# Performance work log

Measured on AMD Instinct MI355X. Metric: run time of the kernel, lower is better.

The kernel has to match this reference:

```python
import jax, jax.numpy as jnp
import numpy as np
import math

FACTOR = 5

def setup_inputs() -> dict:
    key = jax.random.key(0)
    k1, k2, k3, k4 = jax.random.split(key, 4)
    B, L, H, D = 4, 4096, 8, 64
    sample_k = min(FACTOR * int(np.ceil(np.log(L))), L)  # 45
    return {
        "queries": jax.random.normal(k1, (B, L, H, D), dtype=jnp.float32),
        "keys": jax.random.normal(k2, (B, L, H, D), dtype=jnp.float32),
        "values": jax.random.normal(k3, (B, L, H, D), dtype=jnp.float32),
        "index_sample": jax.random.randint(k4, (L, sample_k), 0, L, dtype=jnp.int64),
    }

def reference(queries, keys, values, index_sample):
    # [B, L, H, D] -> [B, H, L, D]
    Q = jnp.transpose(queries, (0, 2, 1, 3))
    K = jnp.transpose(keys, (0, 2, 1, 3))
    V = jnp.transpose(values, (0, 2, 1, 3))
    b, h, l_q, d = Q.shape
    l_k = K.shape[2]

    # n_top (u) per Informer: factor * ceil(ln(l_q)), capped at l_q
    u = min(FACTOR * int(math.ceil(math.log(l_q))), l_q)

    # --- _prob_QK: sampled QK scores ---
    # K_sample: [b, h, l_q, sample_k, d] via shared per-query random sample
    K_sample = K[:, :, index_sample, :]
    # Q_K_sample: [b, h, l_q, sample_k]
    Q_K_sample = jnp.einsum("bhqd,bhqsd->bhqs", Q, K_sample)
    # sparsity measure M: max - mean(sum/l_k)
    M = Q_K_sample.max(axis=-1) - Q_K_sample.sum(axis=-1) / l_k
    # top-u queries (indices; order irrelevant to the math)
    _, M_top = jax.lax.top_k(M, u)  # [b, h, u]

    # Q_reduce: [b, h, u, d]
    Q_reduce = jnp.take_along_axis(Q, M_top[..., None], axis=2)
    # full scores for selected queries: [b, h, u, l_k]
    scale = 1.0 / math.sqrt(d)
    scores_top = jnp.einsum("bhud,bhkd->bhuk", Q_reduce, K) * scale

    # --- initial context: mean of V broadcast over queries ---
    context = jnp.broadcast_to(V.mean(axis=2, keepdims=True), (b, h, l_q, d))

    # --- update context at selected query positions ---
    attn = jax.nn.softmax(scores_top, axis=-1)          # [b, h, u, l_k]
    upd = jnp.einsum("bhuk,bhkd->bhud", attn, V)         # [b, h, u, d]
    bi = jnp.arange(b)[:, None, None]
    hi = jnp.arange(h)[None, :, None]
    context = context.at[bi, hi, M_top].set(upd)

    # [B, H, L, D] -> [B, L, H, D]
    return jnp.transpose(context, (0, 2, 1, 3))
```

## Files before the change

kernel.cpp:

```cpp
#include <hip/hip_runtime.h>
#include <stdint.h>

#define B_ 4
#define L_ 4096
#define H_ 8
#define D_ 64
#define S_ 45
#define U_ 45
#define BH_ 32
#define KC_ 16
#define STRIDE_ (H_*D_)
#define BSTR_ ((size_t)L_*H_*D_)

__device__ __forceinline__ bool detect_idx64(const int* idxp){
    bool z = true;
    #pragma unroll
    for (int i = 1; i < 32; i += 2) z = z && (idxp[i] == 0);
    return z;
}

typedef float v4f_ __attribute__((ext_vector_type(4)));
__device__ __forceinline__ float4 ntload4(const float4* p){
    v4f_ v = __builtin_nontemporal_load((const v4f_*)p);
    return make_float4(v.x, v.y, v.z, v.w);
}
__device__ __forceinline__ void ntstore4(float4* p, float4 f){
    v4f_ v; v.x = f.x; v.y = f.y; v.z = f.z; v.w = f.w;
    __builtin_nontemporal_store(v, (v4f_*)p);
}

__global__ __launch_bounds__(256) void kM(const float* __restrict__ Qb,
                                          const float* __restrict__ Kb,
                                          const int* __restrict__ idxp,
                                          float* __restrict__ Mout){
    int g = blockIdx.x;
    int grp8 = g & 7;
    int b  = grp8 >> 1;
    int hg = grp8 & 1;
    int chunk = g >> 3;
    int q0 = chunk * 16;
    bool idx64 = detect_idx64(idxp);

    __shared__ int lidx[16*S_];
    for (int i = threadIdx.x; i < 16*S_; i += 256)
        lidx[i] = idx64 ? __builtin_nontemporal_load(&idxp[2*(q0*S_ + i)])
                        : __builtin_nontemporal_load(&idxp[q0*S_ + i]);
    __syncthreads();

    int lane = threadIdx.x & 63;
    int w    = threadIdx.x >> 6;
    int grp  = lane >> 4;
    int l16  = lane & 15;
    int ql   = w*4 + grp;
    int q    = q0 + ql;

    const float4* qr = (const float4*)(Qb + (size_t)b*BSTR_ + (size_t)q*STRIDE_ + hg*256);
    float4 qf0 = ntload4(qr + l16);
    float4 qf1 = ntload4(qr + 16 + l16);
    float4 qf2 = ntload4(qr + 32 + l16);
    float4 qf3 = ntload4(qr + 48 + l16);

    const float* kbase = Kb + (size_t)b*BSTR_ + hg*256;
    float mxa = -1e30f, mxb = -1e30f, sma = 0.f, smb = 0.f;
    const int* myIdx = &lidx[ql*S_];

    #pragma unroll 3
    for (int s = 0; s < S_; s++){
        int ki = myIdx[s];
        const float4* kr = (const float4*)(kbase + (size_t)ki*STRIDE_);
        float4 k0 = kr[l16], k1 = kr[16+l16], k2 = kr[32+l16], k3 = kr[48+l16];
        float p0 = qf0.x*k0.x; p0 = fmaf(qf0.y,k0.y,p0); p0 = fmaf(qf0.z,k0.z,p0); p0 = fmaf(qf0.w,k0.w,p0);
        float p1 = qf1.x*k1.x; p1 = fmaf(qf1.y,k1.y,p1); p1 = fmaf(qf1.z,k1.z,p1); p1 = fmaf(qf1.w,k1.w,p1);
        float p2 = qf2.x*k2.x; p2 = fmaf(qf2.y,k2.y,p2); p2 = fmaf(qf2.z,k2.z,p2); p2 = fmaf(qf2.w,k2.w,p2);
        float p3 = qf3.x*k3.x; p3 = fmaf(qf3.y,k3.y,p3); p3 = fmaf(qf3.z,k3.z,p3); p3 = fmaf(qf3.w,k3.w,p3);
        float u0 = p0 + __shfl_xor(p0, 8);
        float u1 = p1 + __shfl_xor(p1, 8);
        float u2 = p2 + __shfl_xor(p2, 8);
        float u3 = p3 + __shfl_xor(p3, 8);
        float va = (l16 < 8) ? u0 : u2;
        float vb = (l16 < 8) ? u1 : u3;
        #pragma unroll
        for (int off = 1; off < 8; off <<= 1){
            va += __shfl_xor(va, off);
            vb += __shfl_xor(vb, off);
        }
        mxa = fmaxf(mxa, va); sma += va;
        mxb = fmaxf(mxb, vb); smb += vb;
    }
    int hsel = (l16==0) ? 0 : (l16==1) ? 1 : (l16==8) ? 2 : (l16==9) ? 3 : -1;
    if (hsel >= 0){
        float mv = (l16 & 1) ? mxb : mxa;
        float sv = (l16 & 1) ? smb : sma;
        __builtin_nontemporal_store(mv - sv*(1.0f/L_),
            &Mout[(size_t)(b*8 + hg*4 + hsel)*L_ + q]);
    }
}

__global__ __launch_bounds__(512) void kTopF(const float* __restrict__ M,
                                             int* __restrict__ Mtop,
                                             float* __restrict__ meanZ,
                                             unsigned short* __restrict__ selRow16){
    int bh = blockIdx.x;
    int t = threadIdx.x;
    if (t < 64) meanZ[bh*64 + t] = 0.f;
    for (int j = t; j < L_; j += 512) selRow16[(size_t)bh*L_ + j] = 0;

    __shared__ float cV[8*U_];
    __shared__ int   cI[8*U_];
    int wv = t >> 6, lane = t & 63;
    const float* Mr = M + (size_t)bh*L_ + wv*512;
    float v[8];
    #pragma unroll
    for (int j = 0; j < 8; j++) v[j] = Mr[lane + 64*j];

    for (int it = 0; it < U_; it++){
        float best = -1e30f; int bidx = 0x7fffffff;
        #pragma unroll
        for (int j = 0; j < 8; j++){
            int id = lane + 64*j;
            if (v[j] > best){ best = v[j]; bidx = id; }
        }
        #pragma unroll
        for (int off = 1; off < 64; off <<= 1){
            float ov = __shfl_xor(best, off); int oi = __shfl_xor(bidx, off);
            if (ov > best || (ov == best && oi < bidx)){ best = ov; bidx = oi; }
        }
        if (lane == 0){ cV[wv*U_ + it] = best; cI[wv*U_ + it] = wv*512 + bidx; }
        if (lane == (bidx & 63)) v[bidx >> 6] = -1e30f;
    }
    __syncthreads();
    if (t < 64){
        float v2[6]; int id2[6];
        #pragma unroll
        for (int j = 0; j < 6; j++){
            int slot = t + 64*j;
            if (slot < 8*U_){ v2[j] = cV[slot]; id2[j] = cI[slot]; }
            else            { v2[j] = -1e30f;  id2[j] = 0x7fffffff; }
        }
        for (int it = 0; it < U_; it++){
            float best = -1e30f; int bidx = 0x7fffffff; int bj = 0;
            #pragma unroll
            for (int j = 0; j < 6; j++){
                if (v2[j] > best || (v2[j] == best && id2[j] < bidx)){
                    best = v2[j]; bidx = id2[j]; bj = j;
                }
            }
            float myBest = best; int myIdx = bidx;
            #pragma unroll
            for (int off = 1; off < 64; off <<= 1){
                float ov = __shfl_xor(best, off); int oi = __shfl_xor(bidx, off);
                if (ov > best || (ov == best && oi < bidx)){ best = ov; bidx = oi; }
            }
            if (t == 0){
                Mtop[bh*U_ + it] = bidx;
                selRow16[(size_t)bh*L_ + bidx] = (unsigned short)(it + 1);
            }
            if (myBest == best && myIdx == bidx) v2[bj] = -1e30f;
        }
    }
}

__global__ __launch_bounds__(256) void kAttnPart(const float* __restrict__ Qb,
                                                 const float* __restrict__ Kb,
                                                 const float* __restrict__ Vb,
                                                 const int*   __restrict__ Mtop,
                                                 float* __restrict__ Opart,
                                                 float* __restrict__ mlG,
                                                 float* __restrict__ mean){
    int bh = blockIdx.y, b = bh >> 3, h = bh & 7;
    int kc = blockIdx.x, uh = blockIdx.z;
    int u0 = uh ? 23 : 0;
    int nu = uh ? 22 : 23;
    int t = threadIdx.x;
    __shared__ float S[24][260];
    __shared__ int   qidx[23];

    if (t < nu) qidx[t] = Mtop[bh*U_ + u0 + t];
    for (int i = t; i < (24 - nu)*260; i += 256) (&S[nu][0])[i] = 0.f;
    __syncthreads();

    int k = kc*256 + t;
    float4 kf[16];
    const float4* K4 = (const float4*)(Kb + (size_t)b*BSTR_ + (size_t)k*STRIDE_ + h*D_);
    #pragma unroll
    for (int c = 0; c < 16; c++) kf[c] = K4[c];
    for (int u = 0; u < nu; u++){
        int qi = __builtin_amdgcn_readfirstlane(qidx[u]);
        const float4* qp = (const float4*)(Qb + (size_t)b*BSTR_ + (size_t)qi*STRIDE_ + h*D_);
        float a0=0.f, a1=0.f, a2=0.f, a3=0.f;
        #pragma unroll
        for (int c = 0; c < 16; c++){
            float4 qv = qp[c];
            a0 = fmaf(qv.x, kf[c].x, a0);
            a1 = fmaf(qv.y, kf[c].y, a1);
            a2 = fmaf(qv.z, kf[c].z, a2);
            a3 = fmaf(qv.w, kf[c].w, a3);
        }
        S[u][t] = ((a0+a1)+(a2+a3)) * 0.125f;
    }
    __syncthreads();

    int wv = t >> 6, lane = t & 63;
    for (int u = wv; u < nu; u += 4){
        float4 sv = *(const float4*)&S[u][lane*4];
        float m = fmaxf(fmaxf(sv.x, sv.y), fmaxf(sv.z, sv.w));
        #pragma unroll
        for (int off = 1; off < 64; off <<= 1) m = fmaxf(m, __shfl_xor(m, off));
        float e0 = __expf(sv.x - m), e1 = __expf(sv.y - m);
        float e2 = __expf(sv.z - m), e3 = __expf(sv.w - m);
        float ls = (e0+e1)+(e2+e3);
        #pragma unroll
        for (int off = 1; off < 64; off <<= 1) ls += __shfl_xor(ls, off);
        float4 pv; pv.x = e0; pv.y = e1; pv.z = e2; pv.w = e3;
        *(float4*)&S[u][lane*4] = pv;
        if (lane == 0){
            size_t mi = ((size_t)(bh*KC_ + kc)*U_ + u0 + u)*2;
            mlG[mi] = m; mlG[mi+1] = ls;
        }
    }
    __syncthreads();

    int d = lane, w = wv;
    int ub = w*6;
    int nuw = nu - ub; if (nuw > 6) nuw = 6; if (nuw < 0) nuw = 0;
    float acc[6];
    #pragma unroll
    for (int j = 0; j < 6; j++) acc[j] = 0.f;
    float vsum = 0.f;
    const float* Vbase = Vb + (size_t)b*BSTR_ + (size_t)(kc*256)*STRIDE_ + h*D_ + d;
    for (int kb = 0; kb < 64; kb++){
        float v0 = Vbase[(size_t)(kb*4+0)*STRIDE_];
        float v1 = Vbase[(size_t)(kb*4+1)*STRIDE_];
        float v2 = Vbase[(size_t)(kb*4+2)*STRIDE_];
        float v3 = Vbase[(size_t)(kb*4+3)*STRIDE_];
        if (uh == 0 && w == 0) vsum += (v0+v1)+(v2+v3);
        #pragma unroll
        for (int j = 0; j < 6; j++){
            float4 p = *(const float4*)&S[ub+j][kb*4];
            acc[j] = fmaf(p.x, v0, acc[j]);
            acc[j] = fmaf(p.y, v1, acc[j]);
            acc[j] = fmaf(p.z, v2, acc[j]);
            acc[j] = fmaf(p.w, v3, acc[j]);
        }
    }
    for (int j = 0; j < nuw; j++)
        Opart[((size_t)(bh*KC_ + kc)*U_ + u0 + ub + j)*64 + d] = acc[j];
    if (uh == 0 && w == 0)
        atomicAdd(&mean[bh*64 + d], vsum);
}

__global__ __launch_bounds__(256) void kOut(const float* __restrict__ mean,
                                            const unsigned short* __restrict__ selRow16,
                                            const float* __restrict__ mlG,
                                            const float* __restrict__ Opart,
                                            float* __restrict__ out){
    size_t t = (size_t)blockIdx.x*256 + threadIdx.x;
    int d16 = (int)(t & 15); int h = (int)((t >> 4) & 7);
    int l   = (int)((t >> 7) & 4095); int b = (int)(t >> 19);
    int bh = b*8 + h;
    int sel = selRow16[(size_t)bh*L_ + l];
    float4 o;
    if (sel == 0){
        o = *(const float4*)(mean + bh*64 + d16*4);
        const float inv = 1.0f / L_;
        o.x *= inv; o.y *= inv; o.z *= inv; o.w *= inv;
    } else {
        int u = sel - 1;
        float mstar = -1e30f;
        #pragma unroll
        for (int kc = 0; kc < KC_; kc++)
            mstar = fmaxf(mstar, mlG[((size_t)(bh*KC_ + kc)*U_ + u)*2]);
        float lsum = 0.f;
        float4 acc; acc.x = acc.y = acc.z = acc.w = 0.f;
        #pragma unroll
        for (int kc = 0; kc < KC_; kc++){
            size_t mi = ((size_t)(bh*KC_ + kc)*U_ + u)*2;
            float wgt = __expf(mlG[mi] - mstar);
            lsum = fmaf(mlG[mi+1], wgt, lsum);
            float4 op = *(const float4*)(Opart + ((size_t)(bh*KC_ + kc)*U_ + u)*64 + d16*4);
            acc.x = fmaf(wgt, op.x, acc.x);
            acc.y = fmaf(wgt, op.y, acc.y);
            acc.z = fmaf(wgt, op.z, acc.z);
            acc.w = fmaf(wgt, op.w, acc.w);
        }
        float inv = 1.0f / lsum;
        acc.x *= inv; acc.y *= inv; acc.z *= inv; acc.w *= inv;
        o = acc;
    }
    ntstore4(((float4*)out) + t, o);
}

extern "C" void kernel_launch(void* const* d_in, const int* in_sizes, int n_in,
                              void* d_out, int out_size, void* d_ws, size_t ws_size,
                              hipStream_t stream) {
    const float* Qb  = (const float*)d_in[0];
    const float* Kb  = (const float*)d_in[1];
    const float* Vb  = (const float*)d_in[2];
    const int*   idx = (const int*)d_in[3];
    float* out = (float*)d_out;

    float* ws = (float*)d_ws;
    float* M      = ws;
    int*   Mtop   = (int*)(ws + 131072);
    float* mean   = ws + 133120;
    unsigned short* selRow16 = (unsigned short*)(ws + 135168);
    float* mlG    = ws + 266240;
    float* Opart  = ws + 315392;

    kM        <<<dim3(2048),       dim3(256), 0, stream>>>(Qb, Kb, idx, M);
    kTopF     <<<dim3(32),         dim3(512), 0, stream>>>(M, Mtop, mean, selRow16);
    kAttnPart <<<dim3(KC_, 32, 2), dim3(256), 0, stream>>>(Qb, Kb, Vb, Mtop, Opart, mlG, mean);
    kOut      <<<dim3(8192),       dim3(256), 0, stream>>>(mean, selRow16, mlG, Opart, out);
}
```

Baseline: 307.4 us.

## Split top-k into per-segment kernel and parallel rank-based merge

The single 32-block top-k kernel becomes two kernels. First, 256 one-wave blocks each pick the top 45 of a 512-element segment. Second, a merge kernel ranks all 360 candidates in parallel by binary-searching the other sorted lists, replacing the serial 45-iteration wave reduction. This spreads the selection across more CUs and shortens the serial merge, at the cost of an extra launch and a global round trip for the candidates.

Result: faster. 276.8 us (-9.9%).

```diff
diff --git a/kernel.cpp b/kernel.cpp
--- a/kernel.cpp
+++ b/kernel.cpp
@@ -96,66 +96,71 @@
     }
 }
 
-__global__ __launch_bounds__(512) void kTopF(const float* __restrict__ M,
-                                             int* __restrict__ Mtop,
-                                             float* __restrict__ meanZ,
-                                             unsigned short* __restrict__ selRow16){
+__global__ __launch_bounds__(64) void kTopSeg(const float* __restrict__ M,
+                                              float* __restrict__ candV,
+                                              int*   __restrict__ candI,
+                                              unsigned short* __restrict__ selRow16){
+    int g = blockIdx.x;
+    int bh = g >> 3, seg = g & 7;
+    int lane = threadIdx.x;
+    uint4 z; z.x = z.y = z.z = z.w = 0u;
+    ((uint4*)(selRow16 + (size_t)bh*L_ + seg*512))[lane] = z;
+
+    const float* Mr = M + (size_t)bh*L_ + seg*512;
+    float v[8];
+    #pragma unroll
+    for (int j = 0; j < 8; j++) v[j] = Mr[lane + 64*j];
+
+    float* cV = candV + (size_t)g*U_;
+    int*   cI = candI + (size_t)g*U_;
+    for (int it = 0; it < U_; it++){
+        float best = -1e30f; int bidx = 0x7fffffff;
+        #pragma unroll
+        for (int j = 0; j < 8; j++){
+            int id = lane + 64*j;
+            if (v[j] > best){ best = v[j]; bidx = id; }
+        }
+        #pragma unroll
+        for (int off = 1; off < 64; off <<= 1){
+            float ov = __shfl_xor(best, off); int oi = __shfl_xor(bidx, off);
+            if (ov > best || (ov == best && oi < bidx)){ best = ov; bidx = oi; }
+        }
+        if (lane == 0){ cV[it] = best; cI[it] = seg*512 + bidx; }
+        if (lane == (bidx & 63)) v[bidx >> 6] = -1e30f;
+    }
+}
+
+__global__ __launch_bounds__(384) void kTopMerge(const float* __restrict__ candV,
+                                                 const int*   __restrict__ candI,
+                                                 int* __restrict__ Mtop,
+                                                 unsigned short* __restrict__ selRow16,
+                                                 float* __restrict__ meanZ){
     int bh = blockIdx.x;
     int t = threadIdx.x;
     if (t < 64) meanZ[bh*64 + t] = 0.f;
-    for (int j = t; j < L_; j += 512) selRow16[(size_t)bh*L_ + j] = 0;
-
-    __shared__ float cV[8*U_];
-    __shared__ int   cI[8*U_];
-    int wv = t >> 6, lane = t & 63;
-    const float* Mr = M + (size_t)bh*L_ + wv*512;
-    float v[8];
-    #pragma unroll
-    for (int j = 0; j < 8; j++) v[j] = Mr[lane + 64*j];
-
-    for (int it = 0; it < U_; it++){
-        float best = -1e30f; int bidx = 0x7fffffff;
-        #pragma unroll
-        for (int j = 0; j < 8; j++){
-            int id = lane + 64*j;
-            if (v[j] > best){ best = v[j]; bidx = id; }
-        }
-        #pragma unroll
-        for (int off = 1; off < 64; off <<= 1){
-            float ov = __shfl_xor(best, off); int oi = __shfl_xor(bidx, off);
-            if (ov > best || (ov == best && oi < bidx)){ best = ov; bidx = oi; }
-        }
-        if (lane == 0){ cV[wv*U_ + it] = best; cI[wv*U_ + it] = wv*512 + bidx; }
-        if (lane == (bidx & 63)) v[bidx >> 6] = -1e30f;
-    }
-    __syncthreads();
-    if (t < 64){
-        float v2[6]; int id2[6];
-        #pragma unroll
-        for (int j = 0; j < 6; j++){
-            int slot = t + 64*j;
-            if (slot < 8*U_){ v2[j] = cV[slot]; id2[j] = cI[slot]; }
-            else            { v2[j] = -1e30f;  id2[j] = 0x7fffffff; }
-        }
-        for (int it = 0; it < U_; it++){
-            float best = -1e30f; int bidx = 0x7fffffff; int bj = 0;
-            #pragma unroll
-            for (int j = 0; j < 6; j++){
-                if (v2[j] > best || (v2[j] == best && id2[j] < bidx)){
-                    best = v2[j]; bidx = id2[j]; bj = j;
-                }
+    __shared__ float sV[8*U_];
+    __shared__ int   sI[8*U_];
+    if (t < 8*U_){ sV[t] = candV[(size_t)bh*8*U_ + t]; sI[t] = candI[(size_t)bh*8*U_ + t]; }
+    __syncthreads();
+    if (t < 8*U_){
+        int s = t / U_, r = t - s*U_;
+        float v = sV[t]; int gi = sI[t];
+        int rank = r;
+        for (int s2 = 0; s2 < 8; s2++){
+            if (s2 == s) continue;
+            const float* LV = &sV[s2*U_];
+            const int*   LI = &sI[s2*U_];
+            int lo = 0, hi = U_;
+            while (lo < hi){
+                int mid = (lo + hi) >> 1;
+                bool before = (LV[mid] > v) || (LV[mid] == v && LI[mid] < gi);
+                if (before) lo = mid + 1; else hi = mid;
             }
-            float myBest = best; int myIdx = bidx;
-            #pragma unroll
-            for (int off = 1; off < 64; off <<= 1){
-                float ov = __shfl_xor(best, off); int oi = __shfl_xor(bidx, off);
-                if (ov > best || (ov == best && oi < bidx)){ best = ov; bidx = oi; }
-            }
-            if (t == 0){
-                Mtop[bh*U_ + it] = bidx;
-                selRow16[(size_t)bh*L_ + bidx] = (unsigned short)(it + 1);
-            }
-            if (myBest == best && myIdx == bidx) v2[bj] = -1e30f;
+            rank += lo;
+        }
+        if (rank < U_){
+            Mtop[bh*U_ + rank] = gi;
+            selRow16[(size_t)bh*L_ + gi] = (unsigned short)(rank + 1);
         }
     }
 }
@@ -304,11 +309,14 @@
     int*   Mtop   = (int*)(ws + 131072);
     float* mean   = ws + 133120;
     unsigned short* selRow16 = (unsigned short*)(ws + 135168);
+    float* candV  = ws + 200704;
+    int*   candI  = (int*)(ws + 212224);
     float* mlG    = ws + 266240;
     float* Opart  = ws + 315392;
 
     kM        <<<dim3(2048),       dim3(256), 0, stream>>>(Qb, Kb, idx, M);
-    kTopF     <<<dim3(32),         dim3(512), 0, stream>>>(M, Mtop, mean, selRow16);
+    kTopSeg   <<<dim3(256),        dim3(64),  0, stream>>>(M, candV, candI, selRow16);
+    kTopMerge <<<dim3(32),         dim3(384), 0, stream>>>(candV, candI, Mtop, selRow16, mean);
     kAttnPart <<<dim3(KC_, 32, 2), dim3(256), 0, stream>>>(Qb, Kb, Vb, Mtop, Opart, mlG, mean);
     kOut      <<<dim3(8192),       dim3(256), 0, stream>>>(mean, selRow16, mlG, Opart, out);
 }
```
